# Performance work log

Measured on AMD Instinct MI355X. Metric: run time of the kernel, lower is better.

Reference implementation:

```python
import jax, jax.numpy as jnp
import numpy as np

N_SEGMENTS = 50000  # number of destination nodes (index values in [0, N_SEGMENTS))


def setup_inputs() -> dict:
    key = jax.random.key(0)
    k1, k2 = jax.random.split(key)
    input = jax.random.normal(k1, (1600000, 64), dtype=jnp.float32)
    index = jax.random.randint(k2, (1600000,), 0, N_SEGMENTS, dtype=jnp.int64)
    return {"input": input, "index": index}


def reference(input, index):
    # Sum-aggregate rows of `input` grouped by `index`: out[n] = sum_{e: index[e]==n} input[e]
    # Equivalent to the custom loma_sum_aggr forward (scatter-add segmented reduction).
    return jax.ops.segment_sum(input, index, num_segments=N_SEGMENTS)
```

## Files before the change

### kernel.cpp

```cpp
#include <hip/hip_runtime.h>

#define N_SEGMENTS 50000
#define N_ROWS     1600000
#define N_FEAT     64

__global__ void hist_kernel(const int* __restrict__ idx, int* __restrict__ counts) {
    int i = blockIdx.x * 256 + threadIdx.x;
    if (i < N_ROWS) atomicAdd(&counts[idx[i]], 1);
}

__device__ __forceinline__ int wave_incl_scan(int v) {
    int lane = threadIdx.x & 63;
#pragma unroll
    for (int d = 1; d < 64; d <<= 1) {
        int t = __shfl_up(v, d, 64);
        if (lane >= d) v += t;
    }
    return v;
}

__global__ void scan_kernel(const int* __restrict__ counts,
                            int* __restrict__ seg_start,
                            int* __restrict__ cursor) {
    __shared__ int wave_off[16];
    __shared__ int s_carry;
    const int tid  = threadIdx.x;
    const int lane = tid & 63;
    const int wid  = tid >> 6;
    if (tid == 0) s_carry = 0;
    __syncthreads();

    for (int base = 0; base < N_SEGMENTS; base += 1024) {
        int i = base + tid;
        int v = (i < N_SEGMENTS) ? counts[i] : 0;
        int incl = wave_incl_scan(v);
        if (lane == 63) wave_off[wid] = incl;
        __syncthreads();
        if (wid == 0) {
            int ws    = (lane < 16) ? wave_off[lane] : 0;
            int wincl = wave_incl_scan(ws);
            if (lane < 16) wave_off[lane] = wincl - ws;
        }
        __syncthreads();
        int excl = incl - v + wave_off[wid] + s_carry;
        if (i < N_SEGMENTS) { seg_start[i] = excl; cursor[i] = excl; }
        __syncthreads();
        if (tid == 1023) s_carry = excl + v;
        __syncthreads();
    }
    if (tid == 0) seg_start[N_SEGMENTS] = s_carry;
}

__global__ void scatter_kernel(const int* __restrict__ idx,
                               int* __restrict__ cursor,
                               int* __restrict__ rowids) {
    int i = blockIdx.x * 256 + threadIdx.x;
    if (i < N_ROWS) {
        int s = idx[i];
        int p = atomicAdd(&cursor[s], 1);
        rowids[p] = i;
    }
}

__global__ void __launch_bounds__(256)
reduce_kernel(const float* __restrict__ in,
              const int*   __restrict__ rowids,
              const int*   __restrict__ seg_start,
              float*       __restrict__ out) {
    const int wid  = threadIdx.x >> 6;
    const int lane = threadIdx.x & 63;
    const int seg  = blockIdx.x * 4 + wid;
    if (seg >= N_SEGMENTS) return;

    const int beg = seg_start[seg];
    const int end = seg_start[seg + 1];

    float acc = 0.f;
    int r = beg;
    for (; r + 4 <= end; r += 4) {
        int r0 = rowids[r], r1 = rowids[r + 1], r2 = rowids[r + 2], r3 = rowids[r + 3];
        float v0 = in[(long long)r0 * N_FEAT + lane];
        float v1 = in[(long long)r1 * N_FEAT + lane];
        float v2 = in[(long long)r2 * N_FEAT + lane];
        float v3 = in[(long long)r3 * N_FEAT + lane];
        acc += v0; acc += v1; acc += v2; acc += v3;
    }
    for (; r < end; ++r)
        acc += in[(long long)rowids[r] * N_FEAT + lane];

    out[(long long)seg * N_FEAT + lane] = acc;
}

extern "C" void kernel_launch(void* const* d_in, const int* in_sizes, int n_in,
                              void* d_out, int out_size, void* d_ws, size_t ws_size,
                              hipStream_t stream) {
    const float* in  = (const float*)d_in[0];
    const int*   idx = (const int*)d_in[1];
    float*       out = (float*)d_out;

    int* counts    = (int*)d_ws;
    int* seg_start = counts + 50048;
    int* cursor    = seg_start + 50048;
    int* rowids    = cursor + 50048;

    hipMemsetAsync(counts, 0, N_SEGMENTS * sizeof(int), stream);

    const int ROW_BLOCKS = (N_ROWS + 255) / 256;
    hist_kernel   <<<ROW_BLOCKS, 256, 0, stream>>>(idx, counts);
    scan_kernel   <<<1, 1024, 0, stream>>>(counts, seg_start, cursor);
    scatter_kernel<<<ROW_BLOCKS, 256, 0, stream>>>(idx, cursor, rowids);

    const int SEG_BLOCKS = (N_SEGMENTS + 3) / 4;
    reduce_kernel <<<SEG_BLOCKS, 256, 0, stream>>>(in, rowids, seg_start, out);
}
```

Baseline: 786.1 us.

## Vectorize index loads, chunk the scan per thread, float4 gather in reduce

The histogram and scatter kernels now handle four indices per thread through int4 loads, which cuts the thread count and the number of load instructions. The single-block scan stops looping serially over 1024-wide tiles with several barriers each. Instead each thread reduces and then writes a contiguous chunk of 49 counts, so only one block-wide scan is needed. The reduce kernel splits each wave into four sub-groups that each gather a whole row as float4s, then combines them with xor shuffles, giving wider loads and more rows in flight. The chunked scan reads counts with a strided, uncoalesced pattern, and the scatter order into rowids changes, which can alter float summation order.

```diff
diff --git a/kernel.cpp b/kernel.cpp
--- a/kernel.cpp
+++ b/kernel.cpp
@@ -5,9 +5,19 @@
 #define N_FEAT     64
 
 __global__ void hist_kernel(const int* __restrict__ idx, int* __restrict__ counts) {
-    int i = blockIdx.x * 256 + threadIdx.x;
-    if (i < N_ROWS) atomicAdd(&counts[idx[i]], 1);
+    int i = (blockIdx.x * 256 + threadIdx.x) * 4;
+    if (i + 3 < N_ROWS) {
+        int4 v = *(const int4*)(idx + i);
+        atomicAdd(&counts[v.x], 1);
+        atomicAdd(&counts[v.y], 1);
+        atomicAdd(&counts[v.z], 1);
+        atomicAdd(&counts[v.w], 1);
+    } else {
+        for (int k = i; k < N_ROWS; ++k) atomicAdd(&counts[idx[k]], 1);
+    }
 }
+
+#define SCAN_CHUNK 49
 
 __device__ __forceinline__ int wave_incl_scan(int v) {
     int lane = threadIdx.x & 63;
@@ -19,46 +29,58 @@
     return v;
 }
 
-__global__ void scan_kernel(const int* __restrict__ counts,
-                            int* __restrict__ seg_start,
-                            int* __restrict__ cursor) {
-    __shared__ int wave_off[16];
-    __shared__ int s_carry;
+__global__ void __launch_bounds__(1024)
+scan_kernel(const int* __restrict__ counts,
+            int* __restrict__ seg_start,
+            int* __restrict__ cursor) {
+    __shared__ int wave_sums[16];
     const int tid  = threadIdx.x;
     const int lane = tid & 63;
     const int wid  = tid >> 6;
-    if (tid == 0) s_carry = 0;
+    const int base = tid * SCAN_CHUNK;
+
+    int tsum = 0;
+#pragma unroll
+    for (int k = 0; k < SCAN_CHUNK; ++k) {
+        int i = base + k;
+        tsum += (i < N_SEGMENTS) ? counts[i] : 0;
+    }
+    int incl = wave_incl_scan(tsum);
+    if (lane == 63) wave_sums[wid] = incl;
     __syncthreads();
+    if (wid == 0) {
+        int ws    = (lane < 16) ? wave_sums[lane] : 0;
+        int wincl = wave_incl_scan(ws);
+        if (lane < 16) wave_sums[lane] = wincl - ws;
+    }
+    __syncthreads();
+    int run = incl - tsum + wave_sums[wid];
 
-    for (int base = 0; base < N_SEGMENTS; base += 1024) {
-        int i = base + tid;
-        int v = (i < N_SEGMENTS) ? counts[i] : 0;
-        int incl = wave_incl_scan(v);
-        if (lane == 63) wave_off[wid] = incl;
-        __syncthreads();
-        if (wid == 0) {
-            int ws    = (lane < 16) ? wave_off[lane] : 0;
-            int wincl = wave_incl_scan(ws);
-            if (lane < 16) wave_off[lane] = wincl - ws;
+#pragma unroll
+    for (int k = 0; k < SCAN_CHUNK; ++k) {
+        int i = base + k;
+        if (i < N_SEGMENTS) {
+            seg_start[i] = run;
+            cursor[i]    = run;
+            run += counts[i];
         }
-        __syncthreads();
-        int excl = incl - v + wave_off[wid] + s_carry;
-        if (i < N_SEGMENTS) { seg_start[i] = excl; cursor[i] = excl; }
-        __syncthreads();
-        if (tid == 1023) s_carry = excl + v;
-        __syncthreads();
     }
-    if (tid == 0) seg_start[N_SEGMENTS] = s_carry;
+    if (tid == 1023) seg_start[N_SEGMENTS] = run;
 }
 
 __global__ void scatter_kernel(const int* __restrict__ idx,
                                int* __restrict__ cursor,
                                int* __restrict__ rowids) {
-    int i = blockIdx.x * 256 + threadIdx.x;
-    if (i < N_ROWS) {
-        int s = idx[i];
-        int p = atomicAdd(&cursor[s], 1);
-        rowids[p] = i;
+    int i = (blockIdx.x * 256 + threadIdx.x) * 4;
+    if (i + 3 < N_ROWS) {
+        int4 v = *(const int4*)(idx + i);
+        rowids[atomicAdd(&cursor[v.x], 1)] = i;
+        rowids[atomicAdd(&cursor[v.y], 1)] = i + 1;
+        rowids[atomicAdd(&cursor[v.z], 1)] = i + 2;
+        rowids[atomicAdd(&cursor[v.w], 1)] = i + 3;
+    } else {
+        for (int k = i; k < N_ROWS; ++k)
+            rowids[atomicAdd(&cursor[idx[k]], 1)] = k;
     }
 }
 
@@ -75,20 +97,43 @@
     const int beg = seg_start[seg];
     const int end = seg_start[seg + 1];
 
-    float acc = 0.f;
+    const int sub = lane >> 4;
+    const int c4  = lane & 15;
+    const float4* in4 = (const float4*)in;
+
+    float4 acc = make_float4(0.f, 0.f, 0.f, 0.f);
+
     int r = beg;
+    for (; r + 8 <= end; r += 8) {
+        int row0 = rowids[r + sub];
+        int row1 = rowids[r + 4 + sub];
+        float4 v0 = in4[(long long)row0 * 16 + c4];
+        float4 v1 = in4[(long long)row1 * 16 + c4];
+        acc.x += v0.x; acc.y += v0.y; acc.z += v0.z; acc.w += v0.w;
+        acc.x += v1.x; acc.y += v1.y; acc.z += v1.z; acc.w += v1.w;
+    }
     for (; r + 4 <= end; r += 4) {
-        int r0 = rowids[r], r1 = rowids[r + 1], r2 = rowids[r + 2], r3 = rowids[r + 3];
-        float v0 = in[(long long)r0 * N_FEAT + lane];
-        float v1 = in[(long long)r1 * N_FEAT + lane];
-        float v2 = in[(long long)r2 * N_FEAT + lane];
-        float v3 = in[(long long)r3 * N_FEAT + lane];
-        acc += v0; acc += v1; acc += v2; acc += v3;
+        int row = rowids[r + sub];
+        float4 v = in4[(long long)row * 16 + c4];
+        acc.x += v.x; acc.y += v.y; acc.z += v.z; acc.w += v.w;
     }
-    for (; r < end; ++r)
-        acc += in[(long long)rowids[r] * N_FEAT + lane];
+    if (r + sub < end) {
+        int row = rowids[r + sub];
+        float4 v = in4[(long long)row * 16 + c4];
+        acc.x += v.x; acc.y += v.y; acc.z += v.z; acc.w += v.w;
+    }
 
-    out[(long long)seg * N_FEAT + lane] = acc;
+#pragma unroll
+    for (int m = 16; m <= 32; m <<= 1) {
+        acc.x += __shfl_xor(acc.x, m, 64);
+        acc.y += __shfl_xor(acc.y, m, 64);
+        acc.z += __shfl_xor(acc.z, m, 64);
+        acc.w += __shfl_xor(acc.w, m, 64);
+    }
+
+    if (sub == 0) {
+        ((float4*)out)[(long long)seg * 16 + c4] = acc;
+    }
 }
 
 extern "C" void kernel_launch(void* const* d_in, const int* in_sizes, int n_in,
@@ -105,10 +150,10 @@
 
     hipMemsetAsync(counts, 0, N_SEGMENTS * sizeof(int), stream);
 
-    const int ROW_BLOCKS = (N_ROWS + 255) / 256;
-    hist_kernel   <<<ROW_BLOCKS, 256, 0, stream>>>(idx, counts);
+    const int VEC_BLOCKS = (N_ROWS / 4 + 255) / 256;
+    hist_kernel   <<<VEC_BLOCKS, 256, 0, stream>>>(idx, counts);
     scan_kernel   <<<1, 1024, 0, stream>>>(counts, seg_start, cursor);
-    scatter_kernel<<<ROW_BLOCKS, 256, 0, stream>>>(idx, cursor, rowids);
+    scatter_kernel<<<VEC_BLOCKS, 256, 0, stream>>>(idx, cursor, rowids);
 
     const int SEG_BLOCKS = (N_SEGMENTS + 3) / 4;
     reduce_kernel <<<SEG_BLOCKS, 256, 0, stream>>>(in, rowids, seg_start, out);
```

Result: slower. 843.9 us (+7.4%).
